# Kernel optimization log

Measured on AMD Instinct MI355X. Metric: run time of the kernel, lower is better.

Reference implementation:

```python
import jax, jax.numpy as jnp
import numpy as np

NUM_GROUPS = 32
EPS = 1e-5  # torch GroupNorm default


def group_norm(x, gamma, beta):
    # x: [b, c, h, w]
    b, c, h, w = x.shape
    xg = x.reshape(b, NUM_GROUPS, c // NUM_GROUPS, h, w)
    mean = xg.mean(axis=(2, 3, 4), keepdims=True)
    var = xg.var(axis=(2, 3, 4), keepdims=True)
    xg = (xg - mean) * jax.lax.rsqrt(var + EPS)
    x = xg.reshape(b, c, h, w)
    return x * gamma[None, :, None, None] + beta[None, :, None, None]


def conv1x1(x, w, bias):
    # 1x1 conv == channel matmul. x: [b,c,h,w], w: [cout,cin]
    y = jnp.einsum('bchw,dc->bdhw', x, w)
    return y + bias[None, :, None, None]


def setup_inputs() -> dict:
    key = jax.random.key(0)
    ks = jax.random.split(key, 11)
    C = 512
    scale = 1.0 / np.sqrt(C)
    x = jax.random.normal(ks[0], (4, C, 64, 64), dtype=jnp.float32)
    return {
        'x': x,
        'gamma': jnp.ones((C,), jnp.float32),
        'beta': jnp.zeros((C,), jnp.float32),
        'wq': jax.random.uniform(ks[1], (C, C), jnp.float32, -scale, scale),
        'bq': jax.random.uniform(ks[2], (C,), jnp.float32, -scale, scale),
        'wk': jax.random.uniform(ks[3], (C, C), jnp.float32, -scale, scale),
        'bk': jax.random.uniform(ks[4], (C,), jnp.float32, -scale, scale),
        'wv': jax.random.uniform(ks[5], (C, C), jnp.float32, -scale, scale),
        'bv': jax.random.uniform(ks[6], (C,), jnp.float32, -scale, scale),
        'wo': jax.random.uniform(ks[7], (C, C), jnp.float32, -scale, scale),
        'bo': jax.random.uniform(ks[8], (C,), jnp.float32, -scale, scale),
    }


def reference(x, gamma, beta, wq, bq, wk, bk, wv, bv, wo, bo):
    b, c, h, w = x.shape
    h_ = group_norm(x, gamma, beta)
    q = conv1x1(h_, wq, bq).reshape(b, c, h * w)
    k = conv1x1(h_, wk, bk).reshape(b, c, h * w)
    v = conv1x1(h_, wv, bv).reshape(b, c, h * w)
    # scores: [b, hw, hw] -- q^T k scaled by c^-0.5
    scores = jnp.einsum('bcn,bcm->bnm', q, k) * (c ** -0.5)
    attn = jax.nn.softmax(scores, axis=2)
    # h_ = v @ attn^T : [b, c, hw]
    out = jnp.einsum('bcm,bnm->bcn', v, attn).reshape(b, c, h, w)
    return x + conv1x1(out, wo, bo)
```

## Files before the change

### kernel.cpp

```cpp
#include <hip/hip_runtime.h>

typedef __bf16 bf16x8 __attribute__((ext_vector_type(8)));
typedef __bf16 bf16x4 __attribute__((ext_vector_type(4)));
typedef float floatx4 __attribute__((ext_vector_type(4)));

#define AS1(p) ((const __attribute__((address_space(1))) unsigned int*)(p))
#define AS3(p) ((__attribute__((address_space(3))) unsigned int*)(p))

__device__ __forceinline__ void async_cp16(const void* g, void* l) {
  __builtin_amdgcn_global_load_lds(AS1(g), AS3(l), 16, 0, 0);
}

template <bool OUT_F32>
__global__ __launch_bounds__(256, 2) void gemm_bt(
    const __bf16* __restrict__ A, const __bf16* __restrict__ B,
    void* __restrict__ Cv, const float* __restrict__ bias,
    const float* __restrict__ residual, const float* __restrict__ colscale,
    int lda, int ldb, int ldc, long sA, long sB, long sC, long sR, int K,
    int bias_mode, float scale, int swz) {
  __shared__ alignas(16) __bf16 As[128 * 32];
  __shared__ alignas(16) __bf16 Bs[128 * 32];

  const int t = threadIdx.x;
  const int bz = blockIdx.z;
  int bx = blockIdx.x, by = blockIdx.y;
  if (swz) {
    const int xcd = bx & 7, idx = bx >> 3;
    by = xcd + (idx >> 2) * 8;
    bx = idx & 3;
  }
  const int m0 = by * 128;
  const int n0 = bx * 128;

  const __bf16* Ab = A + (size_t)bz * sA;
  const __bf16* Bb = B + (size_t)bz * sB;

  const int sr = t >> 2;
  const int sc = t & 3;
  const __bf16* gA0 = Ab + (size_t)(m0 + sr) * lda + sc * 8;
  const __bf16* gA1 = gA0 + (size_t)64 * lda;
  const __bf16* gB0 = Bb + (size_t)(n0 + sr) * ldb + sc * 8;
  const __bf16* gB1 = gB0 + (size_t)64 * ldb;
  __bf16* lA0 = &As[t * 8];
  __bf16* lA1 = &As[(t + 256) * 8];
  __bf16* lB0 = &Bs[t * 8];
  __bf16* lB1 = &Bs[(t + 256) * 8];

  const int lane = t & 63;
  const int wv = t >> 6;
  const int wm = (wv & 1) * 64;
  const int wn = (wv >> 1) * 64;
  const int l15 = lane & 15;
  const int kg = lane >> 4;

  int aoff[4], boff[4];
#pragma unroll
  for (int i = 0; i < 4; ++i) aoff[i] = (wm + i * 16 + l15) * 32 + kg * 8;
#pragma unroll
  for (int j = 0; j < 4; ++j) boff[j] = (wn + j * 16 + l15) * 32 + kg * 8;

  floatx4 acc[4][4] = {};

  const int KT = K >> 5;
  for (int kt = 0; kt < KT; ++kt) {
    const size_t ko = (size_t)kt * 32;
    async_cp16(gA0 + ko, lA0);
    async_cp16(gA1 + ko, lA1);
    async_cp16(gB0 + ko, lB0);
    async_cp16(gB1 + ko, lB1);
    __syncthreads();
    bf16x8 af[4], bfr[4];
#pragma unroll
    for (int i = 0; i < 4; ++i) af[i] = *(const bf16x8*)&As[aoff[i]];
#pragma unroll
    for (int j = 0; j < 4; ++j) bfr[j] = *(const bf16x8*)&Bs[boff[j]];
#pragma unroll
    for (int i = 0; i < 4; ++i)
#pragma unroll
      for (int j = 0; j < 4; ++j)
        acc[i][j] = __builtin_amdgcn_mfma_f32_16x16x32_bf16(af[i], bfr[j],
                                                            acc[i][j], 0, 0, 0);
    __syncthreads();
  }

  const int r0 = m0 + wm + (kg << 2);
  const int c0 = n0 + wn + l15;
#pragma unroll
  for (int i = 0; i < 4; ++i) {
#pragma unroll
    for (int r = 0; r < 4; ++r) {
      const int row = r0 + i * 16 + r;
      float brow = 0.f;
      if (bias_mode == 1) brow = bias[row];
#pragma unroll
      for (int j = 0; j < 4; ++j) {
        const int col = c0 + j * 16;
        float v = acc[i][j][r];
        if (OUT_F32 && colscale) v *= colscale[(size_t)bz * 4096 + col];
        if (bias_mode == 1) v += brow;
        v *= scale;
        const size_t off = (size_t)row * ldc + col;
        if (OUT_F32) {
          float* Cf = (float*)Cv + (size_t)bz * sC;
          if (residual) v += residual[(size_t)bz * sR + off];
          Cf[off] = v;
        } else {
          __bf16* Cb = (__bf16*)Cv + (size_t)bz * sC;
          Cb[off] = (__bf16)v;
        }
      }
    }
  }
}

__global__ __launch_bounds__(256, 2) void gemm_small(
    const __bf16* __restrict__ A0, const __bf16* __restrict__ B0,
    __bf16* __restrict__ C0, const __bf16* __restrict__ A1,
    const __bf16* __restrict__ B1, __bf16* __restrict__ C1, float scale0) {
  __shared__ alignas(16) __bf16 As[128 * 32];
  __shared__ alignas(16) __bf16 Bs[128 * 32];

  const int t = threadIdx.x;
  const int z = blockIdx.z;
  const __bf16* A = z ? A1 : A0;
  const __bf16* B = z ? B1 : B0;
  __bf16* C = z ? C1 : C0;
  const float scale = z ? 1.0f : scale0;
  const int m0 = blockIdx.y * 128;
  const int n0 = blockIdx.x * 128;

  const int sr = t >> 2;
  const int sc = t & 3;
  const __bf16* gA0 = A + (size_t)(m0 + sr) * 512 + sc * 8;
  const __bf16* gA1 = gA0 + (size_t)64 * 512;
  const __bf16* gB0 = B + (size_t)(n0 + sr) * 512 + sc * 8;
  const __bf16* gB1 = gB0 + (size_t)64 * 512;
  __bf16* lA0 = &As[t * 8];
  __bf16* lA1 = &As[(t + 256) * 8];
  __bf16* lB0 = &Bs[t * 8];
  __bf16* lB1 = &Bs[(t + 256) * 8];

  const int lane = t & 63;
  const int wvv = t >> 6;
  const int wm = (wvv & 1) * 64;
  const int wn = (wvv >> 1) * 64;
  const int l15 = lane & 15;
  const int kg = lane >> 4;

  int aoff[4], boff[4];
#pragma unroll
  for (int i = 0; i < 4; ++i) aoff[i] = (wm + i * 16 + l15) * 32 + kg * 8;
#pragma unroll
  for (int j = 0; j < 4; ++j) boff[j] = (wn + j * 16 + l15) * 32 + kg * 8;

  floatx4 acc[4][4] = {};

  for (int kt = 0; kt < 16; ++kt) {
    const size_t ko = (size_t)kt * 32;
    async_cp16(gA0 + ko, lA0);
    async_cp16(gA1 + ko, lA1);
    async_cp16(gB0 + ko, lB0);
    async_cp16(gB1 + ko, lB1);
    __syncthreads();
    bf16x8 af[4], bfr[4];
#pragma unroll
    for (int i = 0; i < 4; ++i) af[i] = *(const bf16x8*)&As[aoff[i]];
#pragma unroll
    for (int j = 0; j < 4; ++j) bfr[j] = *(const bf16x8*)&Bs[boff[j]];
#pragma unroll
    for (int i = 0; i < 4; ++i)
#pragma unroll
      for (int j = 0; j < 4; ++j)
        acc[i][j] = __builtin_amdgcn_mfma_f32_16x16x32_bf16(af[i], bfr[j],
                                                            acc[i][j], 0, 0, 0);
    __syncthreads();
  }

  const int r0 = m0 + wm + (kg << 2);
  const int c0 = n0 + wn + l15;
#pragma unroll
  for (int i = 0; i < 4; ++i)
#pragma unroll
    for (int r = 0; r < 4; ++r) {
      const int row = r0 + i * 16 + r;
#pragma unroll
      for (int j = 0; j < 4; ++j)
        C[(size_t)row * 512 + c0 + j * 16] = (__bf16)(acc[i][j][r] * scale);
    }
}

__global__ __launch_bounds__(512) void gemm_qk8(
    const __bf16* __restrict__ G, const __bf16* __restrict__ Ht,
    const float* __restrict__ wvec, const float* __restrict__ sred,
    const float* __restrict__ gn2, __bf16* __restrict__ SP,
    float* __restrict__ Lpart) {
  __shared__ alignas(16) __bf16 Ab[3][8192];
  __shared__ alignas(16) __bf16 Bb[3][8192];
  __shared__ float smq[256];
  __shared__ float smf[1024];

  const int t = threadIdx.x;
  const int bz = blockIdx.z;
  const int m0 = blockIdx.x * 256;
  const int n0 = blockIdx.y * 256;
  const long sH = 2097152;

  const __bf16* Gb = G + (size_t)bz * sH;
  const __bf16* Hb = Ht + (size_t)bz * sH;

  const int rbase = ((t >> 5) << 3) + (t & 7);
  const int cc8 = ((t >> 3) & 3) * 8;
  const __bf16* gA = Gb + (size_t)(n0 + rbase) * 512 + cc8;
  const __bf16* gB = Hb + (size_t)(m0 + rbase) * 512 + cc8;

  if (t < 256) {
    smq[t] = sqrtf(gn2[(size_t)bz * 4096 + n0 + t]) * sqrtf(sred[0]) + sred[1];
  }
  __builtin_amdgcn_sched_barrier(0);

  const int lane = t & 63;
  const int wid = t >> 6;
  const int wm = (wid & 1) * 128;
  const int wn = (wid >> 1) * 64;
  const int l15 = lane & 15;
  const int kg = lane >> 4;

  const int lodd = ((l15 >> 3) << 8) + kg * 64 + (l15 & 7) * 8;
  const int abase = wm * 32 + lodd;
  const int bbase = wn * 32 + lodd;

#define QK_STAGE(KT, S)                                       \
  {                                                           \
    const size_t ko = (size_t)(KT) * 32;                      \
    async_cp16(gA + ko, &Ab[S][t * 8]);                       \
    async_cp16(gA + ko + 65536, &Ab[S][4096 + t * 8]);        \
    async_cp16(gB + ko, &Bb[S][t * 8]);                       \
    async_cp16(gB + ko + 65536, &Bb[S][4096 + t * 8]);        \
  }

  floatx4 acc[8][4] = {};
  bf16x8 fa0[8], fb0[4], fa1[8], fb1[4];

  QK_STAGE(0, 0);
  QK_STAGE(1, 1);
  QK_STAGE(2, 2);
  asm volatile("s_waitcnt vmcnt(4)" ::: "memory");
  __builtin_amdgcn_sched_barrier(0);
  __builtin_amdgcn_s_barrier();
#pragma unroll
  for (int i = 0; i < 8; ++i) fa0[i] = *(const bf16x8*)&Ab[0][abase + i * 512];
#pragma unroll
  for (int j = 0; j < 4; ++j) fb0[j] = *(const bf16x8*)&Bb[0][bbase + j * 512];
  asm volatile("s_waitcnt lgkmcnt(0)" ::: "memory");
  __builtin_amdgcn_sched_barrier(0);
  __builtin_amdgcn_s_barrier();

#define QK_BODY(KT, FA, FB, NA, NB)                                         \
  {                                                                         \
    if ((KT) + 3 < 16) QK_STAGE((KT) + 3, ((KT) % 3));                      \
    if ((KT) + 1 < 16) {                                                    \
      const int s_ = ((KT) + 1) % 3;                                        \
      _Pragma("unroll") for (int i = 0; i < 8; ++i) NA[i] =                 \
          *(const bf16x8*)&Ab[s_][abase + i * 512];                         \
      _Pragma("unroll") for (int j = 0; j < 4; ++j) NB[j] =                 \
          *(const bf16x8*)&Bb[s_][bbase + j * 512];                         \
    }                                                                       \
    __builtin_amdgcn_s_setprio(1);                                          \
    _Pragma("unroll") for (int i = 0; i < 8; ++i)                           \
        _Pragma("unroll") for (int j = 0; j < 4; ++j) acc[i][j] =           \
            __builtin_amdgcn_mfma_f32_16x16x32_bf16(FA[i], FB[j],           \
                                                    acc[i][j], 0, 0, 0);    \
    __builtin_amdgcn_s_setprio(0);                                          \
    if ((KT) <= 12)                                                         \
      asm volatile("s_waitcnt vmcnt(4) lgkmcnt(0)" ::: "memory");           \
    else                                                                    \
      asm volatile("s_waitcnt vmcnt(0) lgkmcnt(0)" ::: "memory");           \
    __builtin_amdgcn_sched_barrier(0);                                      \
    __builtin_amdgcn_s_barrier();                                           \
  }

#pragma unroll
  for (int kt = 0; kt < 16; kt += 2) {
    QK_BODY(kt, fa0, fb0, fa1, fb1);
    QK_BODY(kt + 1, fa1, fb1, fa0, fb0);
  }
#undef QK_BODY
#undef QK_STAGE

  float wv4[4];
#pragma unroll
  for (int j = 0; j < 4; ++j)
    wv4[j] = wvec[(size_t)bz * 4096 + m0 + wn + j * 16 + l15];

  __bf16* Sb = SP + (size_t)bz * 16777216;
  const int qn = wid >> 1;
#pragma unroll
  for (int i = 0; i < 8; ++i) {
#pragma unroll
    for (int r = 0; r < 4; ++r) {
      const int rl = wm + i * 16 + (kg << 2) + r;
      const float Mh = smq[rl];
      const size_t rowbase = (size_t)(n0 + rl) * 4096 + m0 + wn;
      float se = 0.f;
#pragma unroll
      for (int j = 0; j < 4; ++j) {
        const float p = __expf(acc[i][j][r] + wv4[j] - Mh);
        se += p;
        Sb[rowbase + j * 16 + l15] = (__bf16)p;
      }
#pragma unroll
      for (int off = 1; off < 16; off <<= 1) se += __shfl_xor(se, off);
      if (l15 == 0) smf[qn * 256 + rl] = se;
    }
  }
  __syncthreads();
  if (t < 256)
    Lpart[((size_t)bz * 4096 + n0 + t) * 16 + blockIdx.x] =
        smf[t] + smf[256 + t] + smf[512 + t] + smf[768 + t];
}

__global__ __launch_bounds__(256) void gnorm_kernel(const __bf16* __restrict__ G,
                                                    float* __restrict__ gn2) {
  const int t = threadIdx.x;
  const int row = blockIdx.x * 4 + (t >> 6);
  const int lane = t & 63;
  const bf16x8 g = *(const bf16x8*)(G + (size_t)row * 512 + lane * 8);
  float n2 = 0.f;
#pragma unroll
  for (int k = 0; k < 8; ++k) {
    const float f = (float)g[k];
    n2 += f * f;
  }
#pragma unroll
  for (int off = 32; off; off >>= 1) n2 += __shfl_down(n2, off);
  if (lane == 0) gn2[row] = n2;
}

__global__ __launch_bounds__(256) void lsum_kernel(const float* __restrict__ Lp,
                                                   float* __restrict__ invL) {
  const int row = blockIdx.x * 256 + threadIdx.x;
  const float* p = Lp + (size_t)row * 16;
  float L = 0.f;
#pragma unroll
  for (int j = 0; j < 16; ++j) L += p[j];
  invL[row] = 1.0f / L;
}

__global__ __launch_bounds__(256) void reduce_kernel(
    const float* __restrict__ hn2, const float* __restrict__ wvec,
    float* __restrict__ sred) {
  const int t = threadIdx.x;
  const floatx4* h4 = (const floatx4*)hn2;
  const floatx4* w4 = (const floatx4*)wvec;
  float mh = 0.f, mw = -1e30f;
  for (int i = t; i < 4096; i += 256) {
    const floatx4 a = h4[i], b = w4[i];
#pragma unroll
    for (int k = 0; k < 4; ++k) {
      mh = fmaxf(mh, a[k]);
      mw = fmaxf(mw, b[k]);
    }
  }
#pragma unroll
  for (int off = 32; off; off >>= 1) {
    mh = fmaxf(mh, __shfl_down(mh, off));
    mw = fmaxf(mw, __shfl_down(mw, off));
  }
  __shared__ float red[8];
  if ((t & 63) == 0) {
    red[t >> 6] = mh;
    red[4 + (t >> 6)] = mw;
  }
  __syncthreads();
  if (t == 0) {
    sred[0] = fmaxf(fmaxf(red[0], red[1]), fmaxf(red[2], red[3]));
    sred[1] = fmaxf(fmaxf(red[4], red[5]), fmaxf(red[6], red[7]));
  }
}

__global__ __launch_bounds__(256) void gn_stats(const float* __restrict__ x,
                                                float* __restrict__ part) {
  const int t = threadIdx.x;
  const size_t base = (size_t)blockIdx.x * 8192;
  const floatx4* xp = (const floatx4*)(x + base);
  float s = 0.f, ss = 0.f;
#pragma unroll
  for (int i = 0; i < 8; ++i) {
    floatx4 v = xp[t + i * 256];
#pragma unroll
    for (int k = 0; k < 4; ++k) {
      s += v[k];
      ss += v[k] * v[k];
    }
  }
#pragma unroll
  for (int off = 32; off; off >>= 1) {
    s += __shfl_down(s, off);
    ss += __shfl_down(ss, off);
  }
  __shared__ float red[8];
  if ((t & 63) == 0) {
    red[t >> 6] = s;
    red[4 + (t >> 6)] = ss;
  }
  __syncthreads();
  if (t == 0) {
    part[blockIdx.x * 2] = red[0] + red[1] + red[2] + red[3];
    part[blockIdx.x * 2 + 1] = red[4] + red[5] + red[6] + red[7];
  }
}

__global__ __launch_bounds__(256) void gn_xform(const float* __restrict__ x,
                                                const float* __restrict__ part,
                                                const float* __restrict__ gamma,
                                                const float* __restrict__ beta,
                                                __bf16* __restrict__ Ht,
                                                __bf16* __restrict__ Hc) {
  __shared__ float tile[64][65];
  __shared__ float lsc[64], lsh[64];
  const int t = threadIdx.x;
  const int b = blockIdx.z;
  const int c0 = blockIdx.y * 64;
  const int n0 = blockIdx.x * 64;

  if (t < 64) {
    const int ch = c0 + t;
    const int bg = b * 32 + (ch >> 4);
    float s = 0.f, ss = 0.f;
#pragma unroll
    for (int k = 0; k < 8; ++k) {
      s += part[(bg * 8 + k) * 2];
      ss += part[(bg * 8 + k) * 2 + 1];
    }
    const float mean = s * (1.f / 65536.f);
    const float var = ss * (1.f / 65536.f) - mean * mean;
    const float rstd = rsqrtf(var + 1e-5f);
    const float g = gamma[ch] * rstd;
    lsc[t] = g;
    lsh[t] = beta[ch] - mean * g;
  }
  __syncthreads();

#pragma unroll
  for (int i = 0; i < 4; ++i) {
    const int slot = i * 256 + t;
    const int c = slot >> 4;
    const int nc = (slot & 15) * 4;
    const int ch = c0 + c;
    const floatx4 v =
        *(const floatx4*)&x[((size_t)b * 512 + ch) * 4096 + n0 + nc];
    const float scl = lsc[c];
    const float shf = lsh[c];
    bf16x4 hv;
#pragma unroll
    for (int k = 0; k < 4; ++k) {
      const float f = v[k] * scl + shf;
      tile[c][nc + k] = f;
      hv[k] = (__bf16)f;
    }
    *(bf16x4*)&Hc[((size_t)b * 512 + ch) * 4096 + n0 + nc] = hv;
  }
  __syncthreads();
#pragma unroll
  for (int i = 0; i < 4; ++i) {
    const int slot = i * 256 + t;
    const int n = slot >> 4;
    const int cc = (slot & 15) * 4;
    bf16x4 o;
#pragma unroll
    for (int k = 0; k < 4; ++k) o[k] = (__bf16)tile[cc + k][n];
    *(bf16x4*)&Ht[((size_t)b * 4096 + n0 + n) * 512 + c0 + cc] = o;
  }
}

__global__ __launch_bounds__(256) void cvt_kernel(const float* w0,
                                                  const float* w1,
                                                  const float* w2,
                                                  const float* w3, __bf16* o0,
                                                  __bf16* o1, __bf16* o2,
                                                  __bf16* o3) {
  __shared__ float tile[64][65];
  const int t = threadIdx.x;
  const int z = blockIdx.z;
  const int r0 = blockIdx.y * 64;
  const int d0 = blockIdx.x * 64;

  if (z == 3) {
#pragma unroll
    for (int i = 0; i < 4; ++i) {
      const int slot = i * 256 + t;
      const int r = slot >> 4;
      const int cc = (slot & 15) * 4;
      const floatx4 v = *(const floatx4*)&w3[(size_t)(r0 + r) * 512 + d0 + cc];
      bf16x4 ov;
#pragma unroll
      for (int k = 0; k < 4; ++k) ov[k] = (__bf16)v[k];
      *(bf16x4*)&o3[(size_t)(r0 + r) * 512 + d0 + cc] = ov;
    }
    return;
  }
  const float* w = z == 0 ? w0 : z == 1 ? w1 : w2;
  __bf16* o = z == 0 ? o0 : z == 1 ? o1 : o2;
#pragma unroll
  for (int i = 0; i < 4; ++i) {
    const int slot = i * 256 + t;
    const int r = slot >> 4;
    const int cc = (slot & 15) * 4;
    const floatx4 v = *(const floatx4*)&w[(size_t)(r0 + r) * 512 + d0 + cc];
#pragma unroll
    for (int k = 0; k < 4; ++k) tile[r][cc + k] = v[k];
  }
  __syncthreads();
#pragma unroll
  for (int i = 0; i < 4; ++i) {
    const int slot = i * 256 + t;
    const int d = slot >> 4;
    const int cc = (slot & 15) * 4;
    bf16x4 ov;
#pragma unroll
    for (int k = 0; k < 4; ++k) ov[k] = (__bf16)tile[cc + k][d];
    *(bf16x4*)&o[(size_t)(d0 + d) * 512 + r0 + cc] = ov;
  }
}

__global__ __launch_bounds__(256) void prep_kernel(
    const float* __restrict__ wk, const float* __restrict__ bq,
    const float* __restrict__ bk, const float* __restrict__ wo,
    const float* __restrict__ bv, const float* __restrict__ bo,
    float* __restrict__ uq, float* __restrict__ bias2, float qscale) {
  const int bidx = blockIdx.x;
  const int t = threadIdx.x;
  float s = 0.f;
  if (bidx < 512) {
    s = bq[t] * wk[(size_t)t * 512 + bidx] +
        bq[t + 256] * wk[(size_t)(t + 256) * 512 + bidx];
  } else if (bidx < 1024) {
    const int d = bidx - 512;
    s = wo[(size_t)d * 512 + t] * bv[t] +
        wo[(size_t)d * 512 + t + 256] * bv[t + 256];
  } else {
    s = bq[t] * bk[t] + bq[t + 256] * bk[t + 256];
  }
#pragma unroll
  for (int off = 32; off; off >>= 1) s += __shfl_down(s, off);
  __shared__ float red[4];
  if ((t & 63) == 0) red[t >> 6] = s;
  __syncthreads();
  if (t == 0) {
    const float tot = red[0] + red[1] + red[2] + red[3];
    if (bidx < 512)
      uq[bidx] = qscale * tot;
    else if (bidx < 1024)
      bias2[bidx - 512] = tot + bo[bidx - 512];
    else
      uq[512] = qscale * tot;
  }
}

__global__ __launch_bounds__(256) void wvec_kernel(const __bf16* __restrict__ Ht,
                                                   const float* __restrict__ uq,
                                                   float* __restrict__ wvec,
                                                   float* __restrict__ hn2) {
  const int t = threadIdx.x;
  const int row = blockIdx.x * 4 + (t >> 6);
  const int lane = t & 63;
  const bf16x8 h = *(const bf16x8*)(Ht + (size_t)row * 512 + lane * 8);
  const floatx4 u0 = *(const floatx4*)(uq + lane * 8);
  const floatx4 u1 = *(const floatx4*)(uq + lane * 8 + 4);
  float s = 0.f, n2 = 0.f;
#pragma unroll
  for (int k = 0; k < 4; ++k) {
    const float f0 = (float)h[k], f1 = (float)h[4 + k];
    s += f0 * u0[k] + f1 * u1[k];
    n2 += f0 * f0 + f1 * f1;
  }
#pragma unroll
  for (int off = 32; off; off >>= 1) {
    s += __shfl_down(s, off);
    n2 += __shfl_down(n2, off);
  }
  if (lane == 0) {
    wvec[row] = s + uq[512];
    hn2[row] = n2;
  }
}

extern "C" void kernel_launch(void* const* d_in, const int* in_sizes, int n_in,
                              void* d_out, int out_size, void* d_ws,
                              size_t ws_size, hipStream_t stream) {
  const float* x = (const float*)d_in[0];
  const float* gamma = (const float*)d_in[1];
  const float* beta = (const float*)d_in[2];
  const float* wq = (const float*)d_in[3];
  const float* bq = (const float*)d_in[4];
  const float* wk = (const float*)d_in[5];
  const float* bk = (const float*)d_in[6];
  const float* wv = (const float*)d_in[7];
  const float* bv = (const float*)d_in[8];
  const float* wo = (const float*)d_in[9];
  const float* bo = (const float*)d_in[10];

  __bf16* ws = (__bf16*)d_ws;
  __bf16* wqT = ws;
  __bf16* wkT = wqT + 262144;
  __bf16* wvT = wkT + 262144;
  __bf16* woB = wvT + 262144;
  __bf16* AqkT = woB + 262144;
  __bf16* Wb = AqkT + 262144;
  __bf16* Ht = Wb + 262144;
  __bf16* Hc = Ht + 8388608;
  __bf16* G = Hc + 8388608;
  __bf16* Z = G + 8388608;
  __bf16* SP = Z + 8388608;
  float* Lpart = (float*)(SP + 67108864);
  float* invL = Lpart + 524288;
  float* hn2 = invL + 16384;
  float* wvec = hn2 + 16384;
  float* uq = wvec + 16384;
  float* bias2 = uq + 1024;
  float* sred = bias2 + 512;
  float* gn2 = sred + 64;
  const size_t need = ((size_t)(6 * 262144 + 4 * 8388608 + 67108864)) * 2 +
                      (524288 + 4 * 16384 + 1024 + 512 + 128) * 4;
  if (ws_size < need) return;

  float* part = (float*)SP;

  const float qscale = 0.04419417382415922f;
  const long sH = 2097152;

  cvt_kernel<<<dim3(8, 8, 4), 256, 0, stream>>>(wq, wk, wv, wo, wqT, wkT, wvT,
                                                woB);
  prep_kernel<<<1025, 256, 0, stream>>>(wk, bq, bk, wo, bv, bo, uq, bias2,
                                        qscale);
  gemm_small<<<dim3(4, 4, 2), 256, 0, stream>>>(wkT, wqT, AqkT, woB, wvT, Wb,
                                                qscale);

  gn_stats<<<1024, 256, 0, stream>>>(x, part);
  gn_xform<<<dim3(64, 8, 4), 256, 0, stream>>>(x, part, gamma, beta, Ht, Hc);

  wvec_kernel<<<4096, 256, 0, stream>>>(Ht, uq, wvec, hn2);

  gemm_bt<false><<<dim3(4, 32, 4), 256, 0, stream>>>(
      Ht, AqkT, G, nullptr, nullptr, nullptr, 512, 512, 512, sH, 0, sH, 0, 512,
      0, 1.0f, 0);

  gnorm_kernel<<<4096, 256, 0, stream>>>(G, gn2);

  reduce_kernel<<<1, 256, 0, stream>>>(hn2, wvec, sred);

  gemm_qk8<<<dim3(16, 16, 4), 512, 0, stream>>>(G, Ht, wvec, sred, gn2, SP,
                                                Lpart);
  lsum_kernel<<<64, 256, 0, stream>>>(Lpart, invL);

  gemm_bt<false><<<dim3(128, 1, 4), 256, 0, stream>>>(
      SP, Hc, Z, nullptr, nullptr, nullptr, 4096, 4096, 512, 16777216, sH, sH,
      0, 4096, 0, 1.0f, 1);

  gemm_bt<true><<<dim3(32, 4, 4), 256, 0, stream>>>(
      Wb, Z, d_out, bias2, x, invL, 512, 512, 4096, 0, sH, sH, sH, 512, 1,
      1.0f, 0);
}
```

Baseline: 414.1 us.

## Split QK^T main loop into two half-tile phases with interleaved A/B staging

Restructures the QK score GEMM K-loop from register double-buffering of whole fragments into two phases per k-step, each loading half the A fragments from LDS and issuing the A or B async global-to-LDS copy for k+2 separately. This lowers fragment register pressure (fa/fa2/fb instead of two full sets) and spreads global loads across phases. In exchange it adds more s_barriers per iteration and drops the LDS-read prefetch overlap with MFMA, so LDS latency may be exposed.

```diff
diff --git a/kernel.cpp b/kernel.cpp
--- a/kernel.cpp
+++ b/kernel.cpp
@@ -229,63 +229,81 @@
   const int abase = wm * 32 + lodd;
   const int bbase = wn * 32 + lodd;
 
-#define QK_STAGE(KT, S)                                       \
-  {                                                           \
-    const size_t ko = (size_t)(KT) * 32;                      \
-    async_cp16(gA + ko, &Ab[S][t * 8]);                       \
-    async_cp16(gA + ko + 65536, &Ab[S][4096 + t * 8]);        \
-    async_cp16(gB + ko, &Bb[S][t * 8]);                       \
-    async_cp16(gB + ko + 65536, &Bb[S][4096 + t * 8]);        \
+#define STAGE_A(KT, S)                                 \
+  {                                                    \
+    const size_t ko = (size_t)(KT) * 32;               \
+    async_cp16(gA + ko, &Ab[S][t * 8]);                \
+    async_cp16(gA + ko + 65536, &Ab[S][4096 + t * 8]); \
+  }
+#define STAGE_B(KT, S)                                 \
+  {                                                    \
+    const size_t ko = (size_t)(KT) * 32;               \
+    async_cp16(gB + ko, &Bb[S][t * 8]);                \
+    async_cp16(gB + ko + 65536, &Bb[S][4096 + t * 8]); \
   }
 
   floatx4 acc[8][4] = {};
-  bf16x8 fa0[8], fb0[4], fa1[8], fb1[4];
-
-  QK_STAGE(0, 0);
-  QK_STAGE(1, 1);
-  QK_STAGE(2, 2);
-  asm volatile("s_waitcnt vmcnt(4)" ::: "memory");
-  __builtin_amdgcn_sched_barrier(0);
+  bf16x8 fa[4], fa2[4], fb[4];
+
+  STAGE_A(0, 0);
+  STAGE_B(0, 0);
+  STAGE_A(1, 1);
+  STAGE_B(1, 1);
+  STAGE_A(2, 2);
+  STAGE_B(2, 2);
+  asm volatile("s_waitcnt vmcnt(8)" ::: "memory");
   __builtin_amdgcn_s_barrier();
-#pragma unroll
-  for (int i = 0; i < 8; ++i) fa0[i] = *(const bf16x8*)&Ab[0][abase + i * 512];
-#pragma unroll
-  for (int j = 0; j < 4; ++j) fb0[j] = *(const bf16x8*)&Bb[0][bbase + j * 512];
-  asm volatile("s_waitcnt lgkmcnt(0)" ::: "memory");
-  __builtin_amdgcn_sched_barrier(0);
-  __builtin_amdgcn_s_barrier();
-
-#define QK_BODY(KT, FA, FB, NA, NB)                                         \
+
+#define QK_PHASE0(KT)                                                       \
   {                                                                         \
-    if ((KT) + 3 < 16) QK_STAGE((KT) + 3, ((KT) % 3));                      \
-    if ((KT) + 1 < 16) {                                                    \
-      const int s_ = ((KT) + 1) % 3;                                        \
-      _Pragma("unroll") for (int i = 0; i < 8; ++i) NA[i] =                 \
-          *(const bf16x8*)&Ab[s_][abase + i * 512];                         \
-      _Pragma("unroll") for (int j = 0; j < 4; ++j) NB[j] =                 \
-          *(const bf16x8*)&Bb[s_][bbase + j * 512];                         \
-    }                                                                       \
+    const int s_ = (KT) % 3;                                                \
+    _Pragma("unroll") for (int i = 0; i < 4; ++i) fa[i] =                   \
+        *(const bf16x8*)&Ab[s_][abase + i * 512];                           \
+    _Pragma("unroll") for (int j = 0; j < 4; ++j) fb[j] =                   \
+        *(const bf16x8*)&Bb[s_][bbase + j * 512];                           \
+    if ((KT) + 2 < 16) STAGE_A((KT) + 2, ((KT) + 2) % 3);                   \
+    __builtin_amdgcn_s_barrier();                                           \
+    asm volatile("s_waitcnt lgkmcnt(0)" ::: "memory");                      \
+    __builtin_amdgcn_sched_barrier(0);                                      \
     __builtin_amdgcn_s_setprio(1);                                          \
-    _Pragma("unroll") for (int i = 0; i < 8; ++i)                           \
+    _Pragma("unroll") for (int i = 0; i < 4; ++i)                           \
         _Pragma("unroll") for (int j = 0; j < 4; ++j) acc[i][j] =           \
-            __builtin_amdgcn_mfma_f32_16x16x32_bf16(FA[i], FB[j],           \
+            __builtin_amdgcn_mfma_f32_16x16x32_bf16(fa[i], fb[j],           \
                                                     acc[i][j], 0, 0, 0);    \
     __builtin_amdgcn_s_setprio(0);                                          \
-    if ((KT) <= 12)                                                         \
-      asm volatile("s_waitcnt vmcnt(4) lgkmcnt(0)" ::: "memory");           \
-    else                                                                    \
-      asm volatile("s_waitcnt vmcnt(0) lgkmcnt(0)" ::: "memory");           \
+    __builtin_amdgcn_s_barrier();                                           \
+  }
+#define QK_PHASE1(KT)                                                       \
+  {                                                                         \
+    const int s_ = (KT) % 3;                                                \
+    _Pragma("unroll") for (int i = 0; i < 4; ++i) fa2[i] =                  \
+        *(const bf16x8*)&Ab[s_][abase + 2048 + i * 512];                    \
+    if ((KT) + 2 < 16) STAGE_B((KT) + 2, ((KT) + 2) % 3);                   \
+    __builtin_amdgcn_s_barrier();                                           \
+    asm volatile("s_waitcnt lgkmcnt(0)" ::: "memory");                      \
     __builtin_amdgcn_sched_barrier(0);                                      \
+    __builtin_amdgcn_s_setprio(1);                                          \
+    _Pragma("unroll") for (int i = 0; i < 4; ++i)                           \
+        _Pragma("unroll") for (int j = 0; j < 4; ++j) acc[4 + i][j] =       \
+            __builtin_amdgcn_mfma_f32_16x16x32_bf16(fa2[i], fb[j],          \
+                                                    acc[4 + i][j], 0, 0, 0); \
+    __builtin_amdgcn_s_setprio(0);                                          \
+    if ((KT) <= 13)                                                         \
+      asm volatile("s_waitcnt vmcnt(4)" ::: "memory");                      \
+    else if ((KT) == 14)                                                    \
+      asm volatile("s_waitcnt vmcnt(0)" ::: "memory");                      \
     __builtin_amdgcn_s_barrier();                                           \
   }
 
 #pragma unroll
-  for (int kt = 0; kt < 16; kt += 2) {
-    QK_BODY(kt, fa0, fb0, fa1, fb1);
-    QK_BODY(kt + 1, fa1, fb1, fa0, fb0);
-  }
-#undef QK_BODY
-#undef QK_STAGE
+  for (int kt = 0; kt < 16; ++kt) {
+    QK_PHASE0(kt);
+    QK_PHASE1(kt);
+  }
+#undef QK_PHASE0
+#undef QK_PHASE1
+#undef STAGE_A
+#undef STAGE_B
 
   float wv4[4];
 #pragma unroll
```

Result: no change. 415.6 us (+0.3%).
